# Optimization experiments

Hardware: AMD Instinct MI355X
Metric: run time of the kernel (lower is better)

Reference implementation:

```python
import jax, jax.numpy as jnp
import numpy as np

B, S, D_MODEL = 4, 4096, 1024
H, KD, F = 16, 64, 256
KERNEL_SCALE = 1.0
NORM = 1.0 / np.sqrt(KD).astype(np.float32)  # 1/sqrt(key_dim)
EPS = 1e-6


def setup_inputs() -> dict:
    key = jax.random.key(0)
    ks = jax.random.split(key, 12)
    s = 0.02
    x = jax.random.normal(ks[0], (B, S, D_MODEL), dtype=jnp.float32)
    Wq = jax.random.normal(ks[1], (D_MODEL, H * KD), dtype=jnp.float32) * s
    bq = jnp.zeros((H * KD,), jnp.float32)
    Wk = jax.random.normal(ks[2], (D_MODEL, H * KD), dtype=jnp.float32) * s
    bk = jnp.zeros((H * KD,), jnp.float32)
    Wv = jax.random.normal(ks[3], (D_MODEL, H * KD), dtype=jnp.float32) * s
    bv = jnp.zeros((H * KD,), jnp.float32)
    # RFF params (non-trainable in original; orthogonal-ish random here)
    rff_W = jax.random.normal(ks[4], (KD, F), dtype=jnp.float32)
    q_, _ = jnp.linalg.qr(rff_W.T)  # (F, KD) -> orthonormal rows subset
    rff_W = q_.T[:KD, :F].astype(jnp.float32)
    rff_b = jax.random.uniform(ks[5], (F,), jnp.float32, 0.0, 2.0 * np.pi)
    Wo = jax.random.normal(ks[6], (H * KD, D_MODEL), dtype=jnp.float32) * s
    bo = jnp.zeros((D_MODEL,), jnp.float32)
    return {"x": x, "Wq": Wq, "bq": bq, "Wk": Wk, "bk": bk, "Wv": Wv,
            "bv": bv, "rff_W": rff_W, "rff_b": rff_b, "Wo": Wo, "bo": bo}


def _split_heads(t):
    # [B, S, H*KD] -> [B, H, S, KD]
    return t.reshape(B, S, H, KD).transpose(0, 2, 1, 3)


def _rff(t, rff_W, rff_b):
    # RandomFourierFeatures: cos((x*scale) @ W + b) * sqrt(2/F)
    proj = jnp.einsum('bhsd,df->bhsf', t * KERNEL_SCALE, rff_W) + rff_b
    return jnp.cos(proj) * np.sqrt(2.0 / F).astype(np.float32)


def reference(x, Wq, bq, Wk, bk, Wv, bv, rff_W, rff_b, Wo, bo):
    q = _split_heads(x @ Wq + bq)  # [B,H,S,KD]
    k = _split_heads(x @ Wk + bk)
    v = _split_heads(x @ Wv + bv)
    q_prime = _rff(q * NORM, rff_W, rff_b)  # [B,H,S,F]
    k_prime = _rff(k * NORM, rff_W, rff_b)
    # Non-causal FAVOR+ linear attention: O(L)
    kv = jnp.einsum('bhsf,bhsd->bhfd', k_prime, v)          # [B,H,F,KD]
    k_sum = jnp.sum(k_prime, axis=2)                         # [B,H,F]
    num = jnp.einsum('bhsf,bhfd->bhsd', q_prime, kv)         # [B,H,S,KD]
    den = jnp.einsum('bhsf,bhf->bhs', q_prime, k_sum)        # [B,H,S]
    out = num / (den + EPS)[..., None]
    out = out.transpose(0, 2, 1, 3).reshape(B, S, H * KD)    # merge heads
    return out @ Wo + bo
```

## Files before the change

kernel.cpp:

```cpp
#include <hip/hip_runtime.h>
#include <hip/hip_bf16.h>
#include <math.h>

#define B_SZ    4
#define S_LEN   4096
#define DMODEL  1024
#define NH      16
#define KDIM    64
#define NF      256
#define NROWS   (B_SZ * S_LEN)
#define NCHUNK  8
#define RFF_SCALE 0.08838834764831845f
#define NORM_Q    0.125f

typedef __attribute__((ext_vector_type(8))) short s8v;
typedef __attribute__((ext_vector_type(4))) float f4v;

static __device__ __forceinline__ unsigned short f2bf(float f) {
  unsigned u = __float_as_uint(f);
  unsigned r = (u + 0x7FFFu + ((u >> 16) & 1u)) >> 16;
  return (unsigned short)r;
}

#define MFMA16(a, b, c) __builtin_amdgcn_mfma_f32_16x16x32_bf16((a), (b), (c), 0, 0, 0)

__device__ __forceinline__ void glds16(const void* g, void* l) {
  __builtin_amdgcn_global_load_lds(
      (const __attribute__((address_space(1))) void*)g,
      (__attribute__((address_space(3))) void*)l, 16, 0, 0);
}

__global__ __launch_bounds__(256) void cast_bf16_kernel(
    const float* __restrict__ src, unsigned short* __restrict__ dst, int n8)
{
  int i = blockIdx.x * 256 + threadIdx.x;
  if (i >= n8) return;
  const float* s = src + (size_t)i * 8;
  float4 a = *(const float4*)s;
  float4 b = *(const float4*)(s + 4);
  union { s8v v; unsigned short u[8]; } o;
  o.u[0]=f2bf(a.x); o.u[1]=f2bf(a.y); o.u[2]=f2bf(a.z); o.u[3]=f2bf(a.w);
  o.u[4]=f2bf(b.x); o.u[5]=f2bf(b.y); o.u[6]=f2bf(b.z); o.u[7]=f2bf(b.w);
  *(s8v*)(dst + (size_t)i * 8) = o.v;
}

__global__ __launch_bounds__(256) void transpose_cast_kernel(
    const float* __restrict__ W, unsigned short* __restrict__ WT)
{
  __shared__ float t[32][33];
  const int k0 = blockIdx.y * 32, n0 = blockIdx.x * 32;
  const int c = threadIdx.x & 31, r4 = threadIdx.x >> 5;
#pragma unroll
  for (int i = 0; i < 4; ++i) {
    int row = r4 + i * 8;
    t[row][c] = W[(size_t)(k0 + row) * 1024 + n0 + c];
  }
  __syncthreads();
#pragma unroll
  for (int i = 0; i < 4; ++i) {
    int row = r4 + i * 8;
    WT[(size_t)(n0 + row) * 1024 + k0 + c] = f2bf(t[c][row]);
  }
}

__global__ __launch_bounds__(256) void prep_rff_kernel(
    const float* __restrict__ rffW, unsigned short* __restrict__ rffWT)
{
  int i = blockIdx.x * 256 + threadIdx.x;
  int f = i >> 6, d = i & 63;
  rffWT[(size_t)f * 64 + d] = f2bf(rffW[(size_t)d * 256 + f] * NORM_Q);
}

template <int OUT_BF16, int QKV_FUSED>
__global__ __launch_bounds__(512, 2) void gemm_bt_kernel(
    const unsigned short* __restrict__ A,
    const unsigned short* __restrict__ BT0,
    const unsigned short* __restrict__ BT1,
    const unsigned short* __restrict__ BT2,
    const float* __restrict__ bias0, const float* __restrict__ bias1,
    const float* __restrict__ bias2,
    void* __restrict__ out0, void* __restrict__ out1, void* __restrict__ out2,
    int M, int N, int K, int NXT)
{
  __shared__ __align__(16) unsigned short As[2][16384];
  __shared__ __align__(16) unsigned short Bs[2][16384];
  const int tid = threadIdx.x;
  const int lane = tid & 63, wave = tid >> 6;

  int wg = blockIdx.x;
  {
    const int nwg = gridDim.x;
    const int q = nwg >> 3, r = nwg & 7;
    const int xcd = wg & 7, pos = wg >> 3;
    wg = (xcd < r ? xcd * (q + 1) : r * (q + 1) + (xcd - r) * q) + pos;
  }
  const int m0 = (wg / NXT) * 256;
  int ngl = (wg % NXT) * 256;
  const unsigned short* BT = BT0;
  const float* bias = bias0;
  void* outp = out0;
  if (QKV_FUSED) {
    int which = ngl >> 10;
    if (which == 1) { BT = BT1; bias = bias1; outp = out1; }
    else if (which == 2) { BT = BT2; bias = bias2; outp = out2; }
    ngl &= 1023;
  }
  const int n0 = ngl;

  const int trow = tid >> 3;
  const int g8 = (((lane & 7) ^ (trow & 7)) * 8);
  const unsigned short* aPtr = A  + (size_t)(m0 + trow) * K + g8;
  const unsigned short* bPtr = BT + (size_t)(n0 + trow) * K + g8;
  const int NT = K >> 6;

  auto STAGE = [&](int ts, int h) {
    if (ts >= NT) return;
    const int buf = ts & 1, half = h >> 1;
    const size_t go = (size_t)half * 128 * K + (size_t)ts * 64;
    if ((h & 1) == 0) {
      unsigned short* lp = &As[buf][half * 8192 + wave * 512];
      glds16(aPtr + go, lp);
      glds16(aPtr + go + (size_t)64 * K, lp + 4096);
    } else {
      unsigned short* lp = &Bs[buf][half * 8192 + wave * 512];
      glds16(bPtr + go, lp);
      glds16(bPtr + go + (size_t)64 * K, lp + 4096);
    }
  };

  const int col = lane & 15, quad = lane >> 4;
  const int wm = (wave >> 2) * 128;
  const int wn = (wave & 3) * 64;
  const int c7 = col & 7;
  const int idxA0 = (wm + col) * 64 + ((quad ^ c7) * 8);
  const int idxA1 = (wm + col) * 64 + (((4 + quad) ^ c7) * 8);
  const int idxB0 = (wn + col) * 64 + ((quad ^ c7) * 8);
  const int idxB1 = (wn + col) * 64 + (((4 + quad) ^ c7) * 8);

  f4v acc[2][4][4];
  const f4v zz = {0.f, 0.f, 0.f, 0.f};
#pragma unroll
  for (int h = 0; h < 2; ++h)
#pragma unroll
    for (int i = 0; i < 4; ++i)
#pragma unroll
      for (int j = 0; j < 4; ++j) acc[h][i][j] = zz;

  STAGE(0, 0); STAGE(0, 1); STAGE(0, 2); STAGE(0, 3);
  STAGE(1, 0); STAGE(1, 1); STAGE(1, 2);
  asm volatile("s_waitcnt vmcnt(6)" ::: "memory");
  __builtin_amdgcn_s_barrier();

  s8v a0[4][2], a1[4][2], b0[2][2], b1[2][2];
  {
    const unsigned short* pA = As[0];
    const unsigned short* pB = Bs[0];
#pragma unroll
    for (int u = 0; u < 2; ++u) {
      b0[u][0] = *(const s8v*)&pB[idxB0 + u * 1024];
      b0[u][1] = *(const s8v*)&pB[idxB1 + u * 1024];
    }
#pragma unroll
    for (int x = 0; x < 4; ++x) {
      a0[x][0] = *(const s8v*)&pA[idxA0 + x * 1024];
      a0[x][1] = *(const s8v*)&pA[idxA1 + x * 1024];
    }
  }

  for (int t = 0; t < NT; ++t) {
    const int buf = t & 1;
    const unsigned short* pA = As[buf];
    const unsigned short* pB = Bs[buf];
    const unsigned short* qA = As[buf ^ 1];
    const unsigned short* qB = Bs[buf ^ 1];

    __builtin_amdgcn_s_barrier();
    asm volatile("s_waitcnt lgkmcnt(0)" ::: "memory");
    __builtin_amdgcn_sched_barrier(0);
#pragma unroll
    for (int u = 0; u < 2; ++u) {
      b1[u][0] = *(const s8v*)&pB[idxB0 + 2048 + u * 1024];
      b1[u][1] = *(const s8v*)&pB[idxB1 + 2048 + u * 1024];
    }
    __builtin_amdgcn_sched_barrier(0);
#pragma unroll
    for (int x = 0; x < 4; ++x) {
      a1[x][0] = *(const s8v*)&pA[idxA0 + 4096 + x * 1024];
      a1[x][1] = *(const s8v*)&pA[idxA1 + 4096 + x * 1024];
    }
    __builtin_amdgcn_sched_barrier(0);
    __builtin_amdgcn_s_setprio(1);
#pragma unroll
    for (int x = 0; x < 4; ++x)
#pragma unroll
      for (int u = 0; u < 2; ++u) {
        acc[0][x][u] = MFMA16(a0[x][0], b0[u][0], acc[0][x][u]);
        acc[0][x][u] = MFMA16(a0[x][1], b0[u][1], acc[0][x][u]);
      }
    __builtin_amdgcn_s_setprio(0);
    __builtin_amdgcn_sched_barrier(0);

    __builtin_amdgcn_s_barrier();
    STAGE(t + 1, 3);
    asm volatile("s_waitcnt lgkmcnt(8)" ::: "memory");
    __builtin_amdgcn_sched_barrier(0);
    __builtin_amdgcn_s_setprio(1);
#pragma unroll
    for (int x = 0; x < 4; ++x)
#pragma unroll
      for (int u = 0; u < 2; ++u) {
        acc[0][x][2 + u] = MFMA16(a0[x][0], b1[u][0], acc[0][x][2 + u]);
        acc[0][x][2 + u] = MFMA16(a0[x][1], b1[u][1], acc[0][x][2 + u]);
      }
    __builtin_amdgcn_s_setprio(0);
    __builtin_amdgcn_sched_barrier(0);

    __builtin_amdgcn_s_barrier();
    STAGE(t + 2, 1);
    asm volatile("s_waitcnt lgkmcnt(0)" ::: "memory");
    __builtin_amdgcn_sched_barrier(0);
    __builtin_amdgcn_s_setprio(1);
#pragma unroll
    for (int x = 0; x < 4; ++x)
#pragma unroll
      for (int u = 0; u < 2; ++u) {
        acc[1][x][2 + u] = MFMA16(a1[x][0], b1[u][0], acc[1][x][2 + u]);
        acc[1][x][2 + u] = MFMA16(a1[x][1], b1[u][1], acc[1][x][2 + u]);
      }
    __builtin_amdgcn_s_setprio(0);
    __builtin_amdgcn_sched_barrier(0);

    __builtin_amdgcn_s_barrier();
    STAGE(t + 2, 0);
    STAGE(t + 2, 2);
    if (t < NT - 2) asm volatile("s_waitcnt vmcnt(6)" ::: "memory");
    else            asm volatile("s_waitcnt vmcnt(0)" ::: "memory");
    __builtin_amdgcn_sched_barrier(0);
    s8v b0n[2][2], a0n[4][2];
#pragma unroll
    for (int u = 0; u < 2; ++u) {
      b0n[u][0] = *(const s8v*)&qB[idxB0 + u * 1024];
      b0n[u][1] = *(const s8v*)&qB[idxB1 + u * 1024];
    }
    __builtin_amdgcn_sched_barrier(0);
#pragma unroll
    for (int x = 0; x < 4; ++x) {
      a0n[x][0] = *(const s8v*)&qA[idxA0 + x * 1024];
      a0n[x][1] = *(const s8v*)&qA[idxA1 + x * 1024];
    }
    __builtin_amdgcn_sched_barrier(0);
    __builtin_amdgcn_s_setprio(1);
#pragma unroll
    for (int x = 0; x < 4; ++x)
#pragma unroll
      for (int u = 0; u < 2; ++u) {
        acc[1][x][u] = MFMA16(a1[x][0], b0[u][0], acc[1][x][u]);
        acc[1][x][u] = MFMA16(a1[x][1], b0[u][1], acc[1][x][u]);
      }
    __builtin_amdgcn_s_setprio(0);
    __builtin_amdgcn_sched_barrier(0);
#pragma unroll
    for (int u = 0; u < 2; ++u) { b0[u][0] = b0n[u][0]; b0[u][1] = b0n[u][1]; }
#pragma unroll
    for (int x = 0; x < 4; ++x) { a0[x][0] = a0n[x][0]; a0[x][1] = a0n[x][1]; }
  }

#pragma unroll
  for (int h = 0; h < 2; ++h) {
#pragma unroll
    for (int i = 0; i < 4; ++i) {
#pragma unroll
      for (int j = 0; j < 4; ++j) {
        int n = n0 + wn + j * 16 + col;
        float bv = bias[n];
#pragma unroll
        for (int r = 0; r < 4; ++r) {
          int m = m0 + wm + h * 64 + i * 16 + quad * 4 + r;
          float v = acc[h][i][j][r] + bv;
          if (OUT_BF16)
            ((unsigned short*)outp)[(size_t)m * N + n] = f2bf(v);
          else
            ((float*)outp)[(size_t)m * N + n] = v;
        }
      }
    }
  }
}

__global__ __launch_bounds__(256) void kv_kernel(
    const unsigned short* __restrict__ kg, const unsigned short* __restrict__ vg,
    const unsigned short* __restrict__ rffWT, const float* __restrict__ rffb,
    float* __restrict__ pkv)
{
  __shared__ __align__(16) unsigned short vT[80 * 72];
  __shared__ __align__(16) unsigned short kps[256 * 72];
  const int bh = blockIdx.x, chunk = blockIdx.y;
  const int b = bh >> 4, h = bh & 15;
  const int tid = threadIdx.x;
  const int lane = tid & 63, wave = tid >> 6;
  const int col = lane & 15, quad = lane >> 4;
  const f4v zz = {0.f, 0.f, 0.f, 0.f};

  s8v wf[2][4];
  float bfv[4];
#pragma unroll
  for (int ks = 0; ks < 2; ++ks)
#pragma unroll
    for (int t = 0; t < 4; ++t)
      wf[ks][t] = *(const s8v*)(rffWT +
          (size_t)(wave * 64 + t * 16 + col) * 64 + ks * 32 + quad * 8);
#pragma unroll
  for (int j = 0; j < 4; ++j) bfv[j] = rffb[wave * 64 + j * 16 + col];

  for (int e = tid; e < 1024; e += 256) {
    int r = 64 + (e >> 6), s = e & 63;
    vT[r * 72 + s] = (r == 64) ? (unsigned short)0x3F80 : (unsigned short)0;
  }

  f4v kvacc[4][5];
#pragma unroll
  for (int i = 0; i < 4; ++i)
#pragma unroll
    for (int j = 0; j < 5; ++j) kvacc[i][j] = zz;

  const int sA = tid & 63,        chA = tid >> 6;
  const int sB = (tid + 256) & 63, chB = (tid + 256) >> 6;

  union U { s8v v; unsigned short u[8]; };
  U v0, v1;
  s8v kf[2][4];
  {
    const int s0 = chunk * 512;
    v0.v = *(const s8v*)(vg + ((size_t)(b * S_LEN + s0 + sA)) * DMODEL + h * KDIM + chA * 8);
    v1.v = *(const s8v*)(vg + ((size_t)(b * S_LEN + s0 + sB)) * DMODEL + h * KDIM + chB * 8);
#pragma unroll
    for (int ks = 0; ks < 2; ++ks)
#pragma unroll
      for (int t = 0; t < 4; ++t)
        kf[ks][t] = *(const s8v*)(kg +
            ((size_t)(b * S_LEN + s0 + t * 16 + col)) * DMODEL + h * KDIM + ks * 32 + quad * 8);
  }

  for (int st = 0; st < 8; ++st) {
    const int s0 = chunk * 512 + st * 64;
    __syncthreads();
#pragma unroll
    for (int j = 0; j < 8; ++j) vT[(chA * 8 + j) * 72 + sA] = v0.u[j];
#pragma unroll
    for (int j = 0; j < 8; ++j) vT[(chB * 8 + j) * 72 + sB] = v1.u[j];
    f4v p[4][4];
#pragma unroll
    for (int i = 0; i < 4; ++i)
#pragma unroll
      for (int j = 0; j < 4; ++j) p[i][j] = zz;
#pragma unroll
    for (int ks = 0; ks < 2; ++ks)
#pragma unroll
      for (int i = 0; i < 4; ++i)
#pragma unroll
        for (int j = 0; j < 4; ++j) p[i][j] = MFMA16(kf[ks][i], wf[ks][j], p[i][j]);
    U n0, n1;
    s8v kn[2][4];
    if (st < 7) {
      const int s1 = s0 + 64;
      n0.v = *(const s8v*)(vg + ((size_t)(b * S_LEN + s1 + sA)) * DMODEL + h * KDIM + chA * 8);
      n1.v = *(const s8v*)(vg + ((size_t)(b * S_LEN + s1 + sB)) * DMODEL + h * KDIM + chB * 8);
#pragma unroll
      for (int ks = 0; ks < 2; ++ks)
#pragma unroll
        for (int t = 0; t < 4; ++t)
          kn[ks][t] = *(const s8v*)(kg +
              ((size_t)(b * S_LEN + s1 + t * 16 + col)) * DMODEL + h * KDIM + ks * 32 + quad * 8);
    }
#pragma unroll
    for (int j = 0; j < 4; ++j) {
      int f = wave * 64 + j * 16 + col;
#pragma unroll
      for (int i = 0; i < 4; ++i) {
        union { unsigned long long d; unsigned short u[4]; } pk;
#pragma unroll
        for (int r = 0; r < 4; ++r)
          pk.u[r] = f2bf(__cosf(p[i][j][r] + bfv[j]) * RFF_SCALE);
        *(unsigned long long*)&kps[f * 72 + i * 16 + quad * 4] = pk.d;
      }
    }
    __syncthreads();
#pragma unroll
    for (int ks = 0; ks < 2; ++ks) {
      s8v af[4], bf[5];
#pragma unroll
      for (int t = 0; t < 4; ++t)
        af[t] = *(const s8v*)&kps[(wave * 64 + t * 16 + col) * 72 + ks * 32 + quad * 8];
#pragma unroll
      for (int t = 0; t < 5; ++t)
        bf[t] = *(const s8v*)&vT[(t * 16 + col) * 72 + ks * 32 + quad * 8];
#pragma unroll
      for (int i = 0; i < 4; ++i)
#pragma unroll
        for (int j = 0; j < 5; ++j)
          kvacc[i][j] = MFMA16(af[i], bf[j], kvacc[i][j]);
    }
    v0 = n0; v1 = n1;
#pragma unroll
    for (int ks = 0; ks < 2; ++ks)
#pragma unroll
      for (int t = 0; t < 4; ++t) kf[ks][t] = kn[ks][t];
  }
  const size_t base = ((size_t)(chunk * 64 + bh)) * NF * 80;
#pragma unroll
  for (int i = 0; i < 4; ++i)
#pragma unroll
    for (int r = 0; r < 4; ++r) {
      int f = wave * 64 + i * 16 + quad * 4 + r;
#pragma unroll
      for (int j = 0; j < 5; ++j)
        pkv[base + (size_t)f * 80 + j * 16 + col] = kvacc[i][j][r];
    }
}

__global__ __launch_bounds__(256) void reduce_kv_kernel(
    const float* __restrict__ pkv, unsigned short* __restrict__ kvT)
{
  __shared__ unsigned short lt[80 * 64];
  const int bh = blockIdx.x >> 2, qt = blockIdx.x & 3;
  const int f0 = qt * 64;
  for (int e = threadIdx.x; e < 64 * 80; e += 256) {
    int fl = e / 80, d = e - fl * 80;
    float s = 0.f;
#pragma unroll
    for (int c = 0; c < NCHUNK; ++c)
      s += pkv[((size_t)(c * 64 + bh)) * NF * 80 + (size_t)(f0 + fl) * 80 + d];
    lt[d * 64 + fl] = f2bf(s);
  }
  __syncthreads();
  for (int o = threadIdx.x; o < 80 * 64; o += 256) {
    int d = o >> 6, fl = o & 63;
    kvT[(size_t)bh * 80 * NF + d * 256 + f0 + fl] = lt[o];
  }
}

__global__ __launch_bounds__(256) void attn_kernel(
    const unsigned short* __restrict__ qg, const unsigned short* __restrict__ kvTg,
    const unsigned short* __restrict__ rffWT, const float* __restrict__ rffb,
    unsigned short* __restrict__ att)
{
  __shared__ __align__(16) unsigned short qps[64 * 264];
  __shared__ __align__(16) unsigned short kvs[80 * 264];
  const int bh = blockIdx.x;
  const int b = bh >> 4, h = bh & 15;
  const int tid = threadIdx.x;
  const int lane = tid & 63, wave = tid >> 6;
  const int col = lane & 15, quad = lane >> 4;
  const f4v zz = {0.f, 0.f, 0.f, 0.f};

  s8v wf[2][4];
  float bfv[4];
#pragma unroll
  for (int ks = 0; ks < 2; ++ks)
#pragma unroll
    for (int t = 0; t < 4; ++t)
      wf[ks][t] = *(const s8v*)(rffWT +
          (size_t)(wave * 64 + t * 16 + col) * 64 + ks * 32 + quad * 8);
#pragma unroll
  for (int j = 0; j < 4; ++j) bfv[j] = rffb[wave * 64 + j * 16 + col];

  for (int c = tid; c < 2560; c += 256) {
    int d = c >> 5, ch = c & 31;
    *(s8v*)&kvs[d * 264 + ch * 8] =
        *(const s8v*)(kvTg + (size_t)bh * 80 * NF + d * 256 + ch * 8);
  }

  s8v qf[2][4];
  {
    const int s0 = blockIdx.y * 512;
#pragma unroll
    for (int ks = 0; ks < 2; ++ks)
#pragma unroll
      for (int t = 0; t < 4; ++t)
        qf[ks][t] = *(const s8v*)(qg +
            ((size_t)(b * S_LEN + s0 + t * 16 + col)) * DMODEL + h * KDIM + ks * 32 + quad * 8);
  }

  for (int it = 0; it < 8; ++it) {
    const int s0 = blockIdx.y * 512 + it * 64;
    f4v p[4][4];
#pragma unroll
    for (int i = 0; i < 4; ++i)
#pragma unroll
      for (int j = 0; j < 4; ++j) p[i][j] = zz;
#pragma unroll
    for (int ks = 0; ks < 2; ++ks)
#pragma unroll
      for (int i = 0; i < 4; ++i)
#pragma unroll
        for (int j = 0; j < 4; ++j) p[i][j] = MFMA16(qf[ks][i], wf[ks][j], p[i][j]);
    s8v qn[2][4];
    if (it < 7) {
      const int s1 = s0 + 64;
#pragma unroll
      for (int ks = 0; ks < 2; ++ks)
#pragma unroll
        for (int t = 0; t < 4; ++t)
          qn[ks][t] = *(const s8v*)(qg +
              ((size_t)(b * S_LEN + s1 + t * 16 + col)) * DMODEL + h * KDIM + ks * 32 + quad * 8);
    }
    __syncthreads();
#pragma unroll
    for (int j = 0; j < 4; ++j) {
      int f = wave * 64 + j * 16 + col;
#pragma unroll
      for (int i = 0; i < 4; ++i)
#pragma unroll
        for (int r = 0; r < 4; ++r) {
          int s = i * 16 + quad * 4 + r;
          qps[s * 264 + f] = f2bf(__cosf(p[i][j][r] + bfv[j]) * RFF_SCALE);
        }
    }
    __syncthreads();
    f4v acc[5];
#pragma unroll
    for (int j = 0; j < 5; ++j) acc[j] = zz;
#pragma unroll
    for (int k0 = 0; k0 < 256; k0 += 32) {
      s8v af = *(const s8v*)&qps[(wave * 16 + col) * 264 + k0 + quad * 8];
      s8v bf[5];
#pragma unroll
      for (int t = 0; t < 5; ++t)
        bf[t] = *(const s8v*)&kvs[(t * 16 + col) * 264 + k0 + quad * 8];
#pragma unroll
      for (int j = 0; j < 5; ++j) acc[j] = MFMA16(af, bf[j], acc[j]);
    }
    float inv[4];
#pragma unroll
    for (int r = 0; r < 4; ++r) {
      float den = __shfl(acc[4][r], lane & 48);
      inv[r] = 1.0f / (den + 1e-6f);
    }
#pragma unroll
    for (int r = 0; r < 4; ++r) {
      int m = s0 + wave * 16 + quad * 4 + r;
      size_t obase = ((size_t)(b * S_LEN + m)) * DMODEL + h * KDIM;
#pragma unroll
      for (int j = 0; j < 4; ++j)
        att[obase + j * 16 + col] = f2bf(acc[j][r] * inv[r]);
    }
#pragma unroll
    for (int ks = 0; ks < 2; ++ks)
#pragma unroll
      for (int t = 0; t < 4; ++t) qf[ks][t] = qn[ks][t];
  }
}

extern "C" void kernel_launch(void* const* d_in, const int* in_sizes, int n_in,
                              void* d_out, int out_size, void* d_ws, size_t ws_size,
                              hipStream_t stream)
{
  const float* x    = (const float*)d_in[0];
  const float* Wq   = (const float*)d_in[1];
  const float* bq   = (const float*)d_in[2];
  const float* Wk   = (const float*)d_in[3];
  const float* bk   = (const float*)d_in[4];
  const float* Wv   = (const float*)d_in[5];
  const float* bv   = (const float*)d_in[6];
  const float* rffW = (const float*)d_in[7];
  const float* rffb = (const float*)d_in[8];
  const float* Wo   = (const float*)d_in[9];
  const float* bo   = (const float*)d_in[10];
  float* out = (float*)d_out;

  char* w = (char*)d_ws;
  const size_t XB = (size_t)NROWS * DMODEL * 2;
  const size_t WT = (size_t)DMODEL * DMODEL * 2;
  unsigned short* xb   = (unsigned short*)(w);
  unsigned short* WqT  = (unsigned short*)(w + XB);
  unsigned short* WkT  = (unsigned short*)(w + XB + WT);
  unsigned short* WvT  = (unsigned short*)(w + XB + 2 * WT);
  unsigned short* WoT  = (unsigned short*)(w + XB + 3 * WT);
  unsigned short* rWT  = (unsigned short*)(w + XB + 4 * WT);
  char* p = w + XB + 4 * WT + 65536;
  unsigned short* qb = (unsigned short*)(p);
  unsigned short* kb = (unsigned short*)(p + XB);
  unsigned short* vb = (unsigned short*)(p + 2 * XB);
  float* pkv         = (float*)(p + 3 * XB);
  unsigned short* kvT = (unsigned short*)(p + 3 * XB + (size_t)NCHUNK * 64 * NF * 80 * 4);
  unsigned short* att = kb;

  cast_bf16_kernel<<<NROWS * DMODEL / 8 / 256, 256, 0, stream>>>(x, xb, NROWS * DMODEL / 8);
  dim3 tg(32, 32);
  transpose_cast_kernel<<<tg, 256, 0, stream>>>(Wq, WqT);
  transpose_cast_kernel<<<tg, 256, 0, stream>>>(Wk, WkT);
  transpose_cast_kernel<<<tg, 256, 0, stream>>>(Wv, WvT);
  transpose_cast_kernel<<<tg, 256, 0, stream>>>(Wo, WoT);
  prep_rff_kernel<<<64, 256, 0, stream>>>(rffW, rWT);

  gemm_bt_kernel<1, 1><<<768, 512, 0, stream>>>(
      xb, WqT, WkT, WvT, bq, bk, bv, qb, kb, vb, NROWS, DMODEL, DMODEL, 12);

  kv_kernel<<<dim3(64, NCHUNK), 256, 0, stream>>>(kb, vb, rWT, rffb, pkv);
  reduce_kv_kernel<<<256, 256, 0, stream>>>(pkv, kvT);
  attn_kernel<<<dim3(64, 8), 256, 0, stream>>>(qb, kvT, rWT, rffb, att);

  gemm_bt_kernel<0, 0><<<256, 512, 0, stream>>>(
      att, WoT, nullptr, nullptr, bo, nullptr, nullptr, out, nullptr, nullptr,
      NROWS, DMODEL, DMODEL, 4);
}
```

Before: 404.1 us.

## Switch GEMM to 32x32 MFMA, persistent multi-tile jobs, reorder RFF prefetch

```diff
diff --git a/kernel.cpp b/kernel.cpp
--- a/kernel.cpp
+++ b/kernel.cpp
@@ -15,6 +15,7 @@
 
 typedef __attribute__((ext_vector_type(8))) short s8v;
 typedef __attribute__((ext_vector_type(4))) float f4v;
+typedef __attribute__((ext_vector_type(16))) float f16v;
 
 static __device__ __forceinline__ unsigned short f2bf(float f) {
   unsigned u = __float_as_uint(f);
@@ -23,6 +24,7 @@
 }
 
 #define MFMA16(a, b, c) __builtin_amdgcn_mfma_f32_16x16x32_bf16((a), (b), (c), 0, 0, 0)
+#define MFMA32(a, b, c) __builtin_amdgcn_mfma_f32_32x32x16_bf16((a), (b), (c), 0, 0, 0)
 
 __device__ __forceinline__ void glds16(const void* g, void* l) {
   __builtin_amdgcn_global_load_lds(
@@ -80,38 +82,28 @@
     const float* __restrict__ bias0, const float* __restrict__ bias1,
     const float* __restrict__ bias2,
     void* __restrict__ out0, void* __restrict__ out1, void* __restrict__ out2,
-    int M, int N, int K, int NXT)
+    int M, int N, int K, int NXT, int njobs)
 {
   __shared__ __align__(16) unsigned short As[2][16384];
   __shared__ __align__(16) unsigned short Bs[2][16384];
   const int tid = threadIdx.x;
   const int lane = tid & 63, wave = tid >> 6;
 
-  int wg = blockIdx.x;
+  int p = blockIdx.x;
   {
     const int nwg = gridDim.x;
     const int q = nwg >> 3, r = nwg & 7;
-    const int xcd = wg & 7, pos = wg >> 3;
-    wg = (xcd < r ? xcd * (q + 1) : r * (q + 1) + (xcd - r) * q) + pos;
-  }
-  const int m0 = (wg / NXT) * 256;
-  int ngl = (wg % NXT) * 256;
-  const unsigned short* BT = BT0;
-  const float* bias = bias0;
-  void* outp = out0;
-  if (QKV_FUSED) {
-    int which = ngl >> 10;
-    if (which == 1) { BT = BT1; bias = bias1; outp = out1; }
-    else if (which == 2) { BT = BT2; bias = bias2; outp = out2; }
-    ngl &= 1023;
-  }
-  const int n0 = ngl;
+    const int xcd = p & 7, pos = p >> 3;
+    p = (xcd < r ? xcd * (q + 1) : r * (q + 1) + (xcd - r) * q) + pos;
+  }
+  const int wgbase = p * njobs;
 
   const int trow = tid >> 3;
   const int g8 = (((lane & 7) ^ (trow & 7)) * 8);
-  const unsigned short* aPtr = A  + (size_t)(m0 + trow) * K + g8;
-  const unsigned short* bPtr = BT + (size_t)(n0 + trow) * K + g8;
   const int NT = K >> 6;
+
+  const unsigned short* aPtr;
+  const unsigned short* bPtr;
 
   auto STAGE = [&](int ts, int h) {
     if (ts >= NT) return;
@@ -128,163 +120,190 @@
     }
   };
 
-  const int col = lane & 15, quad = lane >> 4;
+  const int cl = lane & 31, hi = lane >> 5;
   const int wm = (wave >> 2) * 128;
   const int wn = (wave & 3) * 64;
-  const int c7 = col & 7;
-  const int idxA0 = (wm + col) * 64 + ((quad ^ c7) * 8);
-  const int idxA1 = (wm + col) * 64 + (((4 + quad) ^ c7) * 8);
-  const int idxB0 = (wn + col) * 64 + ((quad ^ c7) * 8);
-  const int idxB1 = (wn + col) * 64 + (((4 + quad) ^ c7) * 8);
-
-  f4v acc[2][4][4];
-  const f4v zz = {0.f, 0.f, 0.f, 0.f};
+  const int c7 = cl & 7;
+  int bA[2][2], bB[2], ch8[4];
 #pragma unroll
   for (int h = 0; h < 2; ++h)
 #pragma unroll
-    for (int i = 0; i < 4; ++i)
-#pragma unroll
-      for (int j = 0; j < 4; ++j) acc[h][i][j] = zz;
-
-  STAGE(0, 0); STAGE(0, 1); STAGE(0, 2); STAGE(0, 3);
-  STAGE(1, 0); STAGE(1, 1); STAGE(1, 2);
-  asm volatile("s_waitcnt vmcnt(6)" ::: "memory");
-  __builtin_amdgcn_s_barrier();
-
-  s8v a0[4][2], a1[4][2], b0[2][2], b1[2][2];
-  {
-    const unsigned short* pA = As[0];
-    const unsigned short* pB = Bs[0];
-#pragma unroll
-    for (int u = 0; u < 2; ++u) {
-      b0[u][0] = *(const s8v*)&pB[idxB0 + u * 1024];
-      b0[u][1] = *(const s8v*)&pB[idxB1 + u * 1024];
-    }
-#pragma unroll
-    for (int x = 0; x < 4; ++x) {
-      a0[x][0] = *(const s8v*)&pA[idxA0 + x * 1024];
-      a0[x][1] = *(const s8v*)&pA[idxA1 + x * 1024];
-    }
-  }
-
-  for (int t = 0; t < NT; ++t) {
-    const int buf = t & 1;
-    const unsigned short* pA = As[buf];
-    const unsigned short* pB = Bs[buf];
-    const unsigned short* qA = As[buf ^ 1];
-    const unsigned short* qB = Bs[buf ^ 1];
-
+    for (int rb = 0; rb < 2; ++rb)
+      bA[h][rb] = (wm + h * 64 + rb * 32 + cl) * 64;
+#pragma unroll
+  for (int cb = 0; cb < 2; ++cb) bB[cb] = (wn + cb * 32 + cl) * 64;
+#pragma unroll
+  for (int ks = 0; ks < 4; ++ks) ch8[ks] = (((ks * 2) | hi) ^ c7) * 8;
+
+  f16v acc[2][2][2];
+#pragma unroll
+  for (int h = 0; h < 2; ++h)
+#pragma unroll
+    for (int rb = 0; rb < 2; ++rb)
+#pragma unroll
+      for (int cb = 0; cb < 2; ++cb)
+#pragma unroll
+        for (int e = 0; e < 16; ++e) acc[h][rb][cb][e] = 0.f;
+
+  int pm0 = 0, pn0 = 0;
+  const float* pbias = nullptr;
+  void* poutp = nullptr;
+
+  for (int job = 0; job < njobs; ++job) {
+    const int wge = wgbase + job;
+    const int m0 = (wge / NXT) * 256;
+    int ngl = (wge % NXT) * 256;
+    const unsigned short* BT = BT0;
+    const float* bias = bias0;
+    void* outp = out0;
+    if (QKV_FUSED) {
+      int which = ngl >> 10;
+      if (which == 1) { BT = BT1; bias = bias1; outp = out1; }
+      else if (which == 2) { BT = BT2; bias = bias2; outp = out2; }
+      ngl &= 1023;
+    }
+    const int n0 = ngl;
+    aPtr = A  + (size_t)(m0 + trow) * K + g8;
+    bPtr = BT + (size_t)(n0 + trow) * K + g8;
+
+    if (job > 0) {
+#pragma unroll
+      for (int h = 0; h < 2; ++h)
+#pragma unroll
+        for (int rb = 0; rb < 2; ++rb)
+#pragma unroll
+          for (int cb = 0; cb < 2; ++cb) {
+            int col = pn0 + wn + cb * 32 + cl;
+            float bv = pbias[col];
+            int mB = pm0 + wm + h * 64 + rb * 32;
+#pragma unroll
+            for (int r = 0; r < 16; ++r) {
+              int row = mB + (r & 3) + 8 * (r >> 2) + 4 * hi;
+              float v = acc[h][rb][cb][r] + bv;
+              if (OUT_BF16)
+                ((unsigned short*)poutp)[(size_t)row * N + col] = f2bf(v);
+              else
+                ((float*)poutp)[(size_t)row * N + col] = v;
+            }
+          }
+#pragma unroll
+      for (int h = 0; h < 2; ++h)
+#pragma unroll
+        for (int rb = 0; rb < 2; ++rb)
+#pragma unroll
+          for (int cb = 0; cb < 2; ++cb)
+#pragma unroll
+            for (int e = 0; e < 16; ++e) acc[h][rb][cb][e] = 0.f;
+    }
+
+    STAGE(0, 0); STAGE(0, 1); STAGE(0, 2); STAGE(0, 3);
+    STAGE(1, 0); STAGE(1, 1); STAGE(1, 2);
+    asm volatile("s_waitcnt vmcnt(6)" ::: "memory");
     __builtin_amdgcn_s_barrier();
-    asm volatile("s_waitcnt lgkmcnt(0)" ::: "memory");
-    __builtin_amdgcn_sched_barrier(0);
-#pragma unroll
-    for (int u = 0; u < 2; ++u) {
-      b1[u][0] = *(const s8v*)&pB[idxB0 + 2048 + u * 1024];
-      b1[u][1] = *(const s8v*)&pB[idxB1 + 2048 + u * 1024];
-    }
-    __builtin_amdgcn_sched_barrier(0);
-#pragma unroll
-    for (int x = 0; x < 4; ++x) {
-      a1[x][0] = *(const s8v*)&pA[idxA0 + 4096 + x * 1024];
-      a1[x][1] = *(const s8v*)&pA[idxA1 + 4096 + x * 1024];
-    }
-    __builtin_amdgcn_sched_barrier(0);
-    __builtin_amdgcn_s_setprio(1);
-#pragma unroll
-    for (int x = 0; x < 4; ++x)
-#pragma unroll
-      for (int u = 0; u < 2; ++u) {
-        acc[0][x][u] = MFMA16(a0[x][0], b0[u][0], acc[0][x][u]);
-        acc[0][x][u] = MFMA16(a0[x][1], b0[u][1], acc[0][x][u]);
-      }
-    __builtin_amdgcn_s_setprio(0);
-    __builtin_amdgcn_sched_barrier(0);
-
-    __builtin_amdgcn_s_barrier();
-    STAGE(t + 1, 3);
-    asm volatile("s_waitcnt lgkmcnt(8)" ::: "memory");
-    __builtin_amdgcn_sched_barrier(0);
-    __builtin_amdgcn_s_setprio(1);
-#pragma unroll
-    for (int x = 0; x < 4; ++x)
-#pragma unroll
-      for (int u = 0; u < 2; ++u) {
-        acc[0][x][2 + u] = MFMA16(a0[x][0], b1[u][0], acc[0][x][2 + u]);
-        acc[0][x][2 + u] = MFMA16(a0[x][1], b1[u][1], acc[0][x][2 + u]);
-      }
-    __builtin_amdgcn_s_setprio(0);
-    __builtin_amdgcn_sched_barrier(0);
-
-    __builtin_amdgcn_s_barrier();
-    STAGE(t + 2, 1);
-    asm volatile("s_waitcnt lgkmcnt(0)" ::: "memory");
-    __builtin_amdgcn_sched_barrier(0);
-    __builtin_amdgcn_s_setprio(1);
-#pragma unroll
-    for (int x = 0; x < 4; ++x)
-#pragma unroll
-      for (int u = 0; u < 2; ++u) {
-        acc[1][x][2 + u] = MFMA16(a1[x][0], b1[u][0], acc[1][x][2 + u]);
-        acc[1][x][2 + u] = MFMA16(a1[x][1], b1[u][1], acc[1][x][2 + u]);
-      }
-    __builtin_amdgcn_s_setprio(0);
-    __builtin_amdgcn_sched_barrier(0);
-
-    __builtin_amdgcn_s_barrier();
-    STAGE(t + 2, 0);
-    STAGE(t + 2, 2);
-    if (t < NT - 2) asm volatile("s_waitcnt vmcnt(6)" ::: "memory");
-    else            asm volatile("s_waitcnt vmcnt(0)" ::: "memory");
-    __builtin_amdgcn_sched_barrier(0);
-    s8v b0n[2][2], a0n[4][2];
-#pragma unroll
-    for (int u = 0; u < 2; ++u) {
-      b0n[u][0] = *(const s8v*)&qB[idxB0 + u * 1024];
-      b0n[u][1] = *(const s8v*)&qB[idxB1 + u * 1024];
-    }
-    __builtin_amdgcn_sched_barrier(0);
-#pragma unroll
-    for (int x = 0; x < 4; ++x) {
-      a0n[x][0] = *(const s8v*)&qA[idxA0 + x * 1024];
-      a0n[x][1] = *(const s8v*)&qA[idxA1 + x * 1024];
-    }
-    __builtin_amdgcn_sched_barrier(0);
-    __builtin_amdgcn_s_setprio(1);
-#pragma unroll
-    for (int x = 0; x < 4; ++x)
-#pragma unroll
-      for (int u = 0; u < 2; ++u) {
-        acc[1][x][u] = MFMA16(a1[x][0], b0[u][0], acc[1][x][u]);
-        acc[1][x][u] = MFMA16(a1[x][1], b0[u][1], acc[1][x][u]);
-      }
-    __builtin_amdgcn_s_setprio(0);
-    __builtin_amdgcn_sched_barrier(0);
-#pragma unroll
-    for (int u = 0; u < 2; ++u) { b0[u][0] = b0n[u][0]; b0[u][1] = b0n[u][1]; }
-#pragma unroll
-    for (int x = 0; x < 4; ++x) { a0[x][0] = a0n[x][0]; a0[x][1] = a0n[x][1]; }
-  }
-
-#pragma unroll
-  for (int h = 0; h < 2; ++h) {
-#pragma unroll
-    for (int i = 0; i < 4; ++i) {
-#pragma unroll
-      for (int j = 0; j < 4; ++j) {
-        int n = n0 + wn + j * 16 + col;
-        float bv = bias[n];
-#pragma unroll
-        for (int r = 0; r < 4; ++r) {
-          int m = m0 + wm + h * 64 + i * 16 + quad * 4 + r;
-          float v = acc[h][i][j][r] + bv;
+
+    for (int t = 0; t < NT; ++t) {
+      const int buf = t & 1;
+      const unsigned short* pA = As[buf];
+      const unsigned short* pB = Bs[buf];
+      s8v aF[2][2][4], bF[2][4];
+
+#pragma unroll
+      for (int ks = 0; ks < 4; ++ks)
+        bF[0][ks] = *(const s8v*)&pB[bB[0] + ch8[ks]];
+#pragma unroll
+      for (int rb = 0; rb < 2; ++rb)
+#pragma unroll
+        for (int ks = 0; ks < 4; ++ks)
+          aF[0][rb][ks] = *(const s8v*)&pA[bA[0][rb] + ch8[ks]];
+      STAGE(t + 1, 3);
+      __builtin_amdgcn_s_barrier();
+      asm volatile("s_waitcnt lgkmcnt(0)" ::: "memory");
+      __builtin_amdgcn_sched_barrier(0);
+      __builtin_amdgcn_s_setprio(1);
+#pragma unroll
+      for (int ks = 0; ks < 4; ++ks)
+#pragma unroll
+        for (int rb = 0; rb < 2; ++rb)
+          acc[0][rb][0] = MFMA32(aF[0][rb][ks], bF[0][ks], acc[0][rb][0]);
+      __builtin_amdgcn_s_setprio(0);
+      __builtin_amdgcn_sched_barrier(0);
+      __builtin_amdgcn_s_barrier();
+
+#pragma unroll
+      for (int rb = 0; rb < 2; ++rb)
+#pragma unroll
+        for (int ks = 0; ks < 4; ++ks)
+          aF[1][rb][ks] = *(const s8v*)&pA[bA[1][rb] + ch8[ks]];
+      STAGE(t + 2, 0);
+      __builtin_amdgcn_s_barrier();
+      asm volatile("s_waitcnt lgkmcnt(0)" ::: "memory");
+      __builtin_amdgcn_sched_barrier(0);
+      __builtin_amdgcn_s_setprio(1);
+#pragma unroll
+      for (int ks = 0; ks < 4; ++ks)
+#pragma unroll
+        for (int rb = 0; rb < 2; ++rb)
+          acc[1][rb][0] = MFMA32(aF[1][rb][ks], bF[0][ks], acc[1][rb][0]);
+      __builtin_amdgcn_s_setprio(0);
+      __builtin_amdgcn_sched_barrier(0);
+      __builtin_amdgcn_s_barrier();
+
+#pragma unroll
+      for (int ks = 0; ks < 4; ++ks)
+        bF[1][ks] = *(const s8v*)&pB[bB[1] + ch8[ks]];
+      STAGE(t + 2, 1);
+      __builtin_amdgcn_s_barrier();
+      asm volatile("s_waitcnt lgkmcnt(0)" ::: "memory");
+      __builtin_amdgcn_sched_barrier(0);
+      __builtin_amdgcn_s_setprio(1);
+#pragma unroll
+      for (int ks = 0; ks < 4; ++ks)
+#pragma unroll
+        for (int rb = 0; rb < 2; ++rb)
+          acc[1][rb][1] = MFMA32(aF[1][rb][ks], bF[1][ks], acc[1][rb][1]);
+      __builtin_amdgcn_s_setprio(0);
+      __builtin_amdgcn_sched_barrier(0);
+      __builtin_amdgcn_s_barrier();
+
+      STAGE(t + 2, 2);
+      __builtin_amdgcn_s_barrier();
+      asm volatile("s_waitcnt lgkmcnt(0)" ::: "memory");
+      __builtin_amdgcn_sched_barrier(0);
+      __builtin_amdgcn_s_setprio(1);
+#pragma unroll
+      for (int ks = 0; ks < 4; ++ks)
+#pragma unroll
+        for (int rb = 0; rb < 2; ++rb)
+          acc[0][rb][1] = MFMA32(aF[0][rb][ks], bF[1][ks], acc[0][rb][1]);
+      __builtin_amdgcn_s_setprio(0);
+      __builtin_amdgcn_sched_barrier(0);
+      if (t < NT - 2) asm volatile("s_waitcnt vmcnt(6)" ::: "memory");
+      else            asm volatile("s_waitcnt vmcnt(0)" ::: "memory");
+      __builtin_amdgcn_s_barrier();
+    }
+
+    pm0 = m0; pn0 = n0; pbias = bias; poutp = outp;
+  }
+
+#pragma unroll
+  for (int h = 0; h < 2; ++h)
+#pragma unroll
+    for (int rb = 0; rb < 2; ++rb)
+#pragma unroll
+      for (int cb = 0; cb < 2; ++cb) {
+        int col = pn0 + wn + cb * 32 + cl;
+        float bv = pbias[col];
+        int mB = pm0 + wm + h * 64 + rb * 32;
+#pragma unroll
+        for (int r = 0; r < 16; ++r) {
+          int row = mB + (r & 3) + 8 * (r >> 2) + 4 * hi;
+          float v = acc[h][rb][cb][r] + bv;
           if (OUT_BF16)
-            ((unsigned short*)outp)[(size_t)m * N + n] = f2bf(v);
+            ((unsigned short*)poutp)[(size_t)row * N + col] = f2bf(v);
           else
-            ((float*)outp)[(size_t)m * N + n] = v;
+            ((float*)poutp)[(size_t)row * N + col] = v;
         }
       }
-    }
-  }
 }
 
 __global__ __launch_bounds__(256) void kv_kernel(
@@ -323,7 +342,7 @@
 #pragma unroll
     for (int j = 0; j < 5; ++j) kvacc[i][j] = zz;
 
-  const int sA = tid & 63,        chA = tid >> 6;
+  const int sA = tid & 63,         chA = tid >> 6;
   const int sB = (tid + 256) & 63, chB = (tid + 256) >> 6;
 
   union U { s8v v; unsigned short u[8]; };
@@ -348,17 +367,6 @@
     for (int j = 0; j < 8; ++j) vT[(chA * 8 + j) * 72 + sA] = v0.u[j];
 #pragma unroll
     for (int j = 0; j < 8; ++j) vT[(chB * 8 + j) * 72 + sB] = v1.u[j];
-    f4v p[4][4];
-#pragma unroll
-    for (int i = 0; i < 4; ++i)
-#pragma unroll
-      for (int j = 0; j < 4; ++j) p[i][j] = zz;
-#pragma unroll
-    for (int ks = 0; ks < 2; ++ks)
-#pragma unroll
-      for (int i = 0; i < 4; ++i)
-#pragma unroll
-        for (int j = 0; j < 4; ++j) p[i][j] = MFMA16(kf[ks][i], wf[ks][j], p[i][j]);
     U n0, n1;
     s8v kn[2][4];
     if (st < 7) {
@@ -372,6 +380,17 @@
           kn[ks][t] = *(const s8v*)(kg +
               ((size_t)(b * S_LEN + s1 + t * 16 + col)) * DMODEL + h * KDIM + ks * 32 + quad * 8);
     }
+    f4v p[4][4];
+#pragma unroll
+    for (int i = 0; i < 4; ++i)
+#pragma unroll
+      for (int j = 0; j < 4; ++j) p[i][j] = zz;
+#pragma unroll
+    for (int ks = 0; ks < 2; ++ks)
+#pragma unroll
+      for (int i = 0; i < 4; ++i)
+#pragma unroll
+        for (int j = 0; j < 4; ++j) p[i][j] = MFMA16(kf[ks][i], wf[ks][j], p[i][j]);
 #pragma unroll
     for (int j = 0; j < 4; ++j) {
       int f = wave * 64 + j * 16 + col;
@@ -400,11 +419,13 @@
         for (int j = 0; j < 5; ++j)
           kvacc[i][j] = MFMA16(af[i], bf[j], kvacc[i][j]);
     }
-    v0 = n0; v1 = n1;
-#pragma unroll
-    for (int ks = 0; ks < 2; ++ks)
-#pragma unroll
-      for (int t = 0; t < 4; ++t) kf[ks][t] = kn[ks][t];
+    if (st < 7) {
+      v0 = n0; v1 = n1;
+#pragma unroll
+      for (int ks = 0; ks < 2; ++ks)
+#pragma unroll
+        for (int t = 0; t < 4; ++t) kf[ks][t] = kn[ks][t];
+    }
   }
   const size_t base = ((size_t)(chunk * 64 + bh)) * NF * 80;
 #pragma unroll
@@ -483,17 +504,6 @@
 
   for (int it = 0; it < 8; ++it) {
     const int s0 = blockIdx.y * 512 + it * 64;
-    f4v p[4][4];
-#pragma unroll
-    for (int i = 0; i < 4; ++i)
-#pragma unroll
-      for (int j = 0; j < 4; ++j) p[i][j] = zz;
-#pragma unroll
-    for (int ks = 0; ks < 2; ++ks)
-#pragma unroll
-      for (int i = 0; i < 4; ++i)
-#pragma unroll
-        for (int j = 0; j < 4; ++j) p[i][j] = MFMA16(qf[ks][i], wf[ks][j], p[i][j]);
     s8v qn[2][4];
     if (it < 7) {
       const int s1 = s0 + 64;
@@ -504,6 +514,17 @@
           qn[ks][t] = *(const s8v*)(qg +
               ((size_t)(b * S_LEN + s1 + t * 16 + col)) * DMODEL + h * KDIM + ks * 32 + quad * 8);
     }
+    f4v p[4][4];
+#pragma unroll
+    for (int i = 0; i < 4; ++i)
+#pragma unroll
+      for (int j = 0; j < 4; ++j) p[i][j] = zz;
+#pragma unroll
+    for (int ks = 0; ks < 2; ++ks)
+#pragma unroll
+      for (int i = 0; i < 4; ++i)
+#pragma unroll
+        for (int j = 0; j < 4; ++j) p[i][j] = MFMA16(qf[ks][i], wf[ks][j], p[i][j]);
     __syncthreads();
 #pragma unroll
     for (int j = 0; j < 4; ++j) {
@@ -544,10 +565,12 @@
       for (int j = 0; j < 4; ++j)
         att[obase + j * 16 + col] = f2bf(acc[j][r] * inv[r]);
     }
-#pragma unroll
-    for (int ks = 0; ks < 2; ++ks)
-#pragma unroll
-      for (int t = 0; t < 4; ++t) qf[ks][t] = qn[ks][t];
+    if (it < 7) {
+#pragma unroll
+      for (int ks = 0; ks < 2; ++ks)
+#pragma unroll
+        for (int t = 0; t < 4; ++t) qf[ks][t] = qn[ks][t];
+    }
   }
 }
 
@@ -593,8 +616,8 @@
   transpose_cast_kernel<<<tg, 256, 0, stream>>>(Wo, WoT);
   prep_rff_kernel<<<64, 256, 0, stream>>>(rffW, rWT);
 
-  gemm_bt_kernel<1, 1><<<768, 512, 0, stream>>>(
-      xb, WqT, WkT, WvT, bq, bk, bv, qb, kb, vb, NROWS, DMODEL, DMODEL, 12);
+  gemm_bt_kernel<1, 1><<<256, 512, 0, stream>>>(
+      xb, WqT, WkT, WvT, bq, bk, bv, qb, kb, vb, NROWS, DMODEL, DMODEL, 12, 3);
 
   kv_kernel<<<dim3(64, NCHUNK), 256, 0, stream>>>(kb, vb, rWT, rffb, pkv);
   reduce_kv_kernel<<<256, 256, 0, stream>>>(pkv, kvT);
@@ -602,5 +625,5 @@
 
   gemm_bt_kernel<0, 0><<<256, 512, 0, stream>>>(
       att, WoT, nullptr, nullptr, bo, nullptr, nullptr, out, nullptr, nullptr,
-      NROWS, DMODEL, DMODEL, 4);
-}
+      NROWS, DMODEL, DMODEL, 4, 1);
+}
```

Result: slower. 423.5 us (+4.8%).
